# Optimization experiments

Hardware: AMD Instinct MI355X
Metric: run time of the kernel (lower is better)

Reference implementation:

```python
import jax, jax.numpy as jnp
import numpy as np

EMB = 512       # emb_dim
H = 8           # n_heads
HD = EMB // H   # head_dim = 64
FREQ = 64       # freq_features
PERIOD = 0.1
N = 2048


def setup_inputs() -> dict:
    key = jax.random.key(0)
    ks = jax.random.split(key, 6)
    x = jax.random.normal(ks[0], (1, N, EMB), dtype=jnp.float32)
    v = jax.random.normal(ks[1], (1, N, 3), dtype=jnp.float32)
    vec_map = v / jnp.linalg.norm(v, axis=-1, keepdims=True)  # unit direction vectors
    s_in = 1.0 / np.sqrt(EMB)
    W_qkv = jax.random.normal(ks[2], (EMB, 3 * EMB), dtype=jnp.float32) * s_in
    b_qkv = jnp.zeros((3 * EMB,), dtype=jnp.float32)
    W_bias = jax.random.normal(ks[3], (FREQ, H), dtype=jnp.float32) * (1.0 / np.sqrt(FREQ))
    b_bias = jnp.zeros((H,), dtype=jnp.float32)
    W_out = jax.random.normal(ks[4], (EMB, EMB), dtype=jnp.float32) * s_in
    b_out = jnp.zeros((EMB,), dtype=jnp.float32)
    return {"x": x, "vec_map": vec_map, "W_qkv": W_qkv, "b_qkv": b_qkv,
            "W_bias": W_bias, "b_bias": b_bias, "W_out": W_out, "b_out": b_out}


def reference(x, vec_map, W_qkv, b_qkv, W_bias, b_bias, W_out, b_out):
    batch_dim = x.shape[:-2]
    n = x.shape[-2]
    # QKV projection -> (*, N, H, 3, HD)
    qkv = (x @ W_qkv + b_qkv).reshape(*batch_dim, n, H, 3, HD)
    q, k, v = (qkv[..., 0, :], qkv[..., 1, :], qkv[..., 2, :])
    # attention scores (*, Q, K, H), softmax over the K axis (axis=-2)
    attn = jnp.einsum('...qht,...kht->...qkh', q, k) / np.sqrt(HD)
    attn = jax.nn.softmax(attn, axis=-2)
    # relative bias from pairwise angles between direction vectors
    dot = jnp.einsum('...nc,...mc->...nm', vec_map, vec_map)
    angle = jnp.arccos(jnp.clip(dot, 0.0, 1.0)) / 0.001
    freqs = jnp.linspace(0.0, 1.0, FREQ // 2, dtype=jnp.float32) / PERIOD
    phase = freqs * angle[..., None]                      # (*, N, N, FREQ/2)
    pos = jnp.concatenate((jnp.sin(phase), jnp.cos(phase)), axis=-1)  # (*, N, N, FREQ)
    bias = pos @ W_bias + b_bias                          # (*, N, N, H)
    attn = attn + bias
    # weighted sum of values -> (*, N, EMB)
    y = jnp.einsum('...qkh,...kht->...qht', attn, v).reshape(*batch_dim, n, EMB)
    return y @ W_out + b_out
```

## Files before the change

kernel.cpp:

```cpp
#include <hip/hip_runtime.h>
#include <hip/hip_bf16.h>
#include <math.h>

#define NT 2048
#define EMBD 512
#define NH 8
#define QKV_LD 1536
#define KSPLIT 8

typedef unsigned short u16;
typedef __attribute__((ext_vector_type(8))) short short8;
typedef __attribute__((ext_vector_type(4))) float v4f;

static __device__ __forceinline__ float bf2f(unsigned int u) {
    union { unsigned int i; float f; } c; c.i = u << 16; return c.f;
}
static __device__ __forceinline__ unsigned int f2bf(float x) {
    union { float f; unsigned int u; } c; c.f = x;
    return (c.u + 0x7fffu + ((c.u >> 16) & 1u)) >> 16;
}
static __device__ __forceinline__ unsigned int cvtpk(float lo, float hi) {
    unsigned int r;
    asm("v_cvt_pk_bf16_f32 %0, %1, %2" : "=v"(r) : "v"(lo), "v"(hi));
    return r;
}

__global__ __launch_bounds__(256) void prep(const float* __restrict__ x,
    u16* __restrict__ xh, u16* __restrict__ xl,
    const float* __restrict__ Wqkv, u16* __restrict__ wth, u16* __restrict__ wtl,
    const float* __restrict__ Wout, u16* __restrict__ woth, u16* __restrict__ wotl)
{
    __shared__ float tile[64][65];
    int b = blockIdx.x;
    const int t = threadIdx.x;
    if (b < 1024) {
        int i = (b * 256 + t) << 2;
        float4 v = *(const float4*)(x + i);
        float f[4] = {v.x, v.y, v.z, v.w};
        unsigned int hi[4], lo[4];
#pragma unroll
        for (int j = 0; j < 4; ++j) {
            hi[j] = f2bf(f[j]);
            lo[j] = f2bf(f[j] - bf2f(hi[j]));
        }
        uint2 wh; wh.x = hi[0] | (hi[1] << 16); wh.y = hi[2] | (hi[3] << 16);
        uint2 wl; wl.x = lo[0] | (lo[1] << 16); wl.y = lo[2] | (lo[3] << 16);
        *(uint2*)(xh + i) = wh;
        *(uint2*)(xl + i) = wl;
        return;
    }
    b -= 1024;
    const float* W; u16* th; u16* tl; int ld, bx, by;
    if (b < 192) { W = Wqkv; th = wth;  tl = wtl;  ld = QKV_LD; bx = b % 24; by = b / 24; }
    else { b -= 192; W = Wout; th = woth; tl = wotl; ld = EMBD; bx = b & 7; by = b >> 3; }
    const int n0 = bx << 6, k0 = by << 6;
    const int r = t >> 2, c4 = (t & 3) << 4;
#pragma unroll
    for (int j = 0; j < 4; ++j)
        *(float4*)&tile[r][c4 + (j << 2)] =
            *(const float4*)(W + (size_t)(k0 + r) * ld + n0 + c4 + (j << 2));
    __syncthreads();
    const int n_l = t >> 2;
    u16 vh[16], vl[16];
#pragma unroll
    for (int j = 0; j < 16; ++j) {
        float f = tile[c4 + j][n_l];
        unsigned int h = f2bf(f);
        vh[j] = (u16)h;
        vl[j] = (u16)f2bf(f - bf2f(h));
    }
    u16* dh = th + (size_t)(n0 + n_l) * EMBD + k0 + c4;
    u16* dl = tl + (size_t)(n0 + n_l) * EMBD + k0 + c4;
    *(uint4*)dh       = *(uint4*)&vh[0];
    *(uint4*)(dh + 8) = *(uint4*)&vh[8];
    *(uint4*)dl       = *(uint4*)&vl[0];
    *(uint4*)(dl + 8) = *(uint4*)&vl[8];
}

__global__ __launch_bounds__(256) void gemm_qkv_mfma(const u16* __restrict__ xh,
    const u16* __restrict__ xl, const u16* __restrict__ wth,
    const u16* __restrict__ wtl, const float* __restrict__ bias,
    u16* __restrict__ qkvb)
{
    const int n0 = blockIdx.x << 6, m0 = blockIdx.y << 6;
    const int w = threadIdx.x >> 6, lane = threadIdx.x & 63;
    const int wm = w >> 1, wn = w & 1;
    const int fr = lane & 15, kd = (lane >> 4) << 3;

    const u16* ah0 = xh + (size_t)(m0 + wm * 32 + fr) * EMBD + kd;
    const u16* al0 = xl + (size_t)(m0 + wm * 32 + fr) * EMBD + kd;
    const u16* bh0 = wth + (size_t)(n0 + wn * 32 + fr) * EMBD + kd;
    const u16* bl0 = wtl + (size_t)(n0 + wn * 32 + fr) * EMBD + kd;

    v4f acc[2][2] = {};
    for (int kc = 0; kc < EMBD; kc += 32) {
        short8 a_h[2], a_l[2], b_h[2], b_l[2];
#pragma unroll
        for (int im = 0; im < 2; ++im) {
            a_h[im] = *(const short8*)(ah0 + (size_t)im * 16 * EMBD + kc);
            a_l[im] = *(const short8*)(al0 + (size_t)im * 16 * EMBD + kc);
        }
#pragma unroll
        for (int in = 0; in < 2; ++in) {
            b_h[in] = *(const short8*)(bh0 + (size_t)in * 16 * EMBD + kc);
            b_l[in] = *(const short8*)(bl0 + (size_t)in * 16 * EMBD + kc);
        }
#pragma unroll
        for (int im = 0; im < 2; ++im)
#pragma unroll
            for (int in = 0; in < 2; ++in) {
                acc[im][in] = __builtin_amdgcn_mfma_f32_16x16x32_bf16(a_h[im], b_h[in], acc[im][in], 0, 0, 0);
                acc[im][in] = __builtin_amdgcn_mfma_f32_16x16x32_bf16(a_h[im], b_l[in], acc[im][in], 0, 0, 0);
                acc[im][in] = __builtin_amdgcn_mfma_f32_16x16x32_bf16(a_l[im], b_h[in], acc[im][in], 0, 0, 0);
            }
    }
    const int qr = (lane >> 4) << 2;
#pragma unroll
    for (int im = 0; im < 2; ++im)
#pragma unroll
        for (int in = 0; in < 2; ++in) {
            int n = n0 + wn * 32 + in * 16 + fr;
            float bv = bias[n];
#pragma unroll
            for (int r = 0; r < 4; ++r) {
                int m = m0 + wm * 32 + im * 16 + qr + r;
                qkvb[(size_t)m * QKV_LD + n] = (u16)f2bf(acc[im][in][r] + bv);
            }
        }
}

__global__ __launch_bounds__(256) void transpose_v(const u16* __restrict__ qkvb,
                                                   u16* __restrict__ Vt)
{
    __shared__ u16 tile[64][72];
    const int h = blockIdx.y, k0 = blockIdx.x << 6;
    const int t = threadIdx.x;
    {
        int r = t >> 2, cg = (t & 3) << 4;
        const u16* src = qkvb + (size_t)(k0 + r) * QKV_LD + h * 192 + 128 + cg;
        *(uint4*)&tile[r][cg]     = *(const uint4*)src;
        *(uint4*)&tile[r][cg + 8] = *(const uint4*)(src + 8);
    }
    __syncthreads();
    {
        int c = t >> 2, kg = (t & 3) << 4;
        u16 tmp[16];
#pragma unroll
        for (int j = 0; j < 16; ++j) tmp[j] = tile[kg + j][c];
        u16* dst = Vt + ((size_t)h * 64 + c) * NT + k0 + kg;
        *(uint4*)dst       = *(uint4*)&tmp[0];
        *(uint4*)(dst + 8) = *(uint4*)&tmp[8];
    }
}

__global__ __launch_bounds__(512, 2) void attn_pv(
    const u16* __restrict__ qkvb, const u16* __restrict__ Vt,
    float* __restrict__ zpart, float* __restrict__ partsP)
{
    __shared__ u16 tile[8 * 2056];

    const int bid = blockIdx.x;
    const int zsp = bid & 7;
    const int qt  = bid >> 3;
    const int q0 = qt << 5;
    const int kbase = zsp << 8;

    const int t = threadIdx.x;
    const int w = t >> 6;
    const int lane = t & 63;
    const int fr = lane & 15;
    const int hi4 = lane >> 4;
    const int kd = hi4 << 3;
    const int qr = hi4 << 2;

    short8 aq[2][2];
#pragma unroll
    for (int mb = 0; mb < 2; ++mb)
#pragma unroll
        for (int kk = 0; kk < 2; ++kk)
            aq[mb][kk] = *(const short8*)(qkvb +
                (size_t)(q0 + mb * 16 + fr) * QKV_LD + w * 192 + kk * 32 + kd);

    v4f accP[2][4] = {};
    float zacc[2][4] = {};

    const u16* vsrc = Vt + (size_t)(w * 64 + fr) * NT + kd;
    const u16* ksrc = qkvb + (size_t)fr * QKV_LD + w * 192 + 64 + kd;

#define LOADCH(VB, BK, KC)                                                     \
    _Pragma("unroll")                                                          \
    for (int nt = 0; nt < 4; ++nt)                                             \
        _Pragma("unroll")                                                      \
        for (int kk = 0; kk < 2; ++kk) {                                       \
            VB[nt][kk] = *(const short8*)(vsrc + (size_t)nt * 16 * NT +        \
                                          (KC) + kk * 32);                     \
            BK[nt][kk] = *(const short8*)(ksrc + (size_t)((KC) + nt * 16) *    \
                                          QKV_LD + kk * 32);                   \
        }

#define COMPUTECH(VB, BK)                                                      \
    {                                                                          \
        v4f sacc[2][4] = {};                                                   \
        _Pragma("unroll")                                                      \
        for (int mb = 0; mb < 2; ++mb)                                         \
            _Pragma("unroll")                                                  \
            for (int nt = 0; nt < 4; ++nt) {                                   \
                sacc[mb][nt] = __builtin_amdgcn_mfma_f32_16x16x32_bf16(        \
                    aq[mb][0], BK[nt][0], sacc[mb][nt], 0, 0, 0);              \
                sacc[mb][nt] = __builtin_amdgcn_mfma_f32_16x16x32_bf16(        \
                    aq[mb][1], BK[nt][1], sacc[mb][nt], 0, 0, 0);              \
            }                                                                  \
        unsigned int pk[2][4][2];                                              \
        _Pragma("unroll")                                                      \
        for (int mb = 0; mb < 2; ++mb)                                         \
            _Pragma("unroll")                                                  \
            for (int nt = 0; nt < 4; ++nt)                                     \
                _Pragma("unroll")                                              \
                for (int r2 = 0; r2 < 2; ++r2) {                               \
                    float e0 = __expf(sacc[mb][nt][2 * r2] * 0.125f);          \
                    float e1 = __expf(sacc[mb][nt][2 * r2 + 1] * 0.125f);      \
                    zacc[mb][2 * r2] += e0;                                    \
                    zacc[mb][2 * r2 + 1] += e1;                                \
                    pk[mb][nt][r2] = cvtpk(e0, e1);                            \
                }                                                              \
        _Pragma("unroll")                                                      \
        for (int mb = 0; mb < 2; ++mb)                                         \
            _Pragma("unroll")                                                  \
            for (int nt = 0; nt < 4; ++nt) {                                   \
                const int kg = (nt << 1) + (fr >> 3);                          \
                _Pragma("unroll")                                              \
                for (int r = 0; r < 4; ++r) {                                  \
                    const int q = mb * 16 + qr + r;                            \
                    tile[w * 2056 + q * 64 + ((kg ^ (q & 7)) << 3) +           \
                         (fr & 7)] =                                           \
                        (u16)(pk[mb][nt][r >> 1] >> ((r & 1) << 4));           \
                }                                                              \
            }                                                                  \
        _Pragma("unroll")                                                      \
        for (int mb = 0; mb < 2; ++mb) {                                       \
            const int q = mb * 16 + fr;                                        \
            _Pragma("unroll")                                                  \
            for (int kk = 0; kk < 2; ++kk) {                                   \
                short8 ap = *(const short8*)&tile[w * 2056 + q * 64 +          \
                    (((kk * 4 + hi4) ^ (q & 7)) << 3)];                        \
                _Pragma("unroll")                                              \
                for (int nt = 0; nt < 4; ++nt)                                 \
                    accP[mb][nt] = __builtin_amdgcn_mfma_f32_16x16x32_bf16(    \
                        ap, VB[nt][kk], accP[mb][nt], 0, 0, 0);                \
            }                                                                  \
        }                                                                      \
    }

    short8 v0[4][2], b0[4][2], v1[4][2], b1[4][2];
    LOADCH(v0, b0, kbase)
#pragma unroll
    for (int cc = 0; cc < 2; ++cc) {
        LOADCH(v1, b1, kbase + ((2 * cc + 1) << 6))
        COMPUTECH(v0, b0)
        if (cc < 1) { LOADCH(v0, b0, kbase + ((2 * cc + 2) << 6)) }
        COMPUTECH(v1, b1)
    }
#undef LOADCH
#undef COMPUTECH

#pragma unroll
    for (int off = 1; off < 16; off <<= 1)
#pragma unroll
        for (int mb = 0; mb < 2; ++mb)
#pragma unroll
            for (int r = 0; r < 4; ++r)
                zacc[mb][r] += __shfl_xor(zacc[mb][r], off);
    if (fr == 0) {
#pragma unroll
        for (int mb = 0; mb < 2; ++mb)
#pragma unroll
            for (int r = 0; r < 4; ++r)
                zpart[((size_t)zsp * 8 + w) * NT + q0 + mb * 16 + qr + r] = zacc[mb][r];
    }
    float* pP = partsP + (size_t)zsp * NT * EMBD;
#pragma unroll
    for (int mb = 0; mb < 2; ++mb)
#pragma unroll
        for (int nt = 0; nt < 4; ++nt)
#pragma unroll
            for (int r = 0; r < 4; ++r)
                pP[(size_t)(q0 + mb * 16 + qr + r) * EMBD +
                   (w << 6) + (nt << 4) + fr] = accP[mb][nt][r];
}

__global__ __launch_bounds__(512, 4) void bias_v(
    const u16* __restrict__ Vt, const float* __restrict__ vec,
    const float* __restrict__ Wb, const float* __restrict__ bb,
    float* __restrict__ partsB)
{
    __shared__ float flds[32];
    __shared__ float vql[96];
    __shared__ float ang[32 * 65];
    __shared__ u16 tile[8 * 2056];

    const int bid = blockIdx.x;
    const int zsp = bid & 7;
    const int qt  = bid >> 3;
    const int q0 = qt << 5;
    const int kbase = zsp << 8;

    const int t = threadIdx.x;
    const int w = t >> 6;
    const int lane = t & 63;
    const int fr = lane & 15;
    const int hi4 = lane >> 4;
    const int kd = hi4 << 3;
    const int qr = hi4 << 2;

    if (t < 32) flds[t] = __fdiv_rn(__fdiv_rn((float)t, 31.0f), 0.1f);
    else if (t < 128) vql[t - 32] = vec[q0 * 3 + (t - 32)];

    short8 BS, BC;
#pragma unroll
    for (int j = 0; j < 8; ++j) {
        float ws = (fr < 8) ? Wb[(kd + j) * 8 + fr] : 0.0f;
        float wc = (fr < 8) ? Wb[(32 + kd + j) * 8 + fr] : 0.0f;
        BS[j] = (short)f2bf(ws);
        BC[j] = (short)f2bf(wc);
    }
    const float bbv = (fr < 8) ? bb[fr] : 0.0f;

    v4f accB[2][4] = {};

    __syncthreads();

    for (int c = 0; c < 4; ++c) {
        const int kc = kbase + (c << 6);
        {
            const int p0 = t << 2;
            const int q = p0 >> 6;
            const int kl = p0 & 63;
            const float a0 = vql[q * 3], a1 = vql[q * 3 + 1], a2 = vql[q * 3 + 2];
            const float* vk = vec + (size_t)(kc + kl) * 3;
#pragma unroll
            for (int j = 0; j < 4; ++j) {
                float c0 = vk[j * 3], c1 = vk[j * 3 + 1], c2 = vk[j * 3 + 2];
                float dot = __fadd_rn(__fadd_rn(__fmul_rn(a0, c0), __fmul_rn(a1, c1)),
                                      __fmul_rn(a2, c2));
                float dotc = fminf(fmaxf(dot, 0.0f), 1.0f);
                ang[q * 65 + kl + j] = __fdiv_rn(acosf(dotc), 0.001f);
            }
        }
        __syncthreads();
#pragma unroll
        for (int gi = 0; gi < 16; ++gi) {
            const int g = w + (gi << 3);
            const int q = g >> 2;
            const int ksub = (g & 3) << 4;
            const float av = ang[q * 65 + ksub + fr];
            float sv[8], cv[8];
#pragma unroll
            for (int j = 0; j < 8; ++j) {
                float ph = __fmul_rn(flds[kd + j], av);
                float rv = ph * 0.15915494309189535f;
                float rf = rv - floorf(rv);
                sv[j] = __builtin_amdgcn_sinf(rf);
                cv[j] = __builtin_amdgcn_cosf(rf);
            }
            union { uint4 u; short8 v; } As, Ac;
            As.u.x = cvtpk(sv[0], sv[1]); As.u.y = cvtpk(sv[2], sv[3]);
            As.u.z = cvtpk(sv[4], sv[5]); As.u.w = cvtpk(sv[6], sv[7]);
            Ac.u.x = cvtpk(cv[0], cv[1]); Ac.u.y = cvtpk(cv[2], cv[3]);
            Ac.u.z = cvtpk(cv[4], cv[5]); Ac.u.w = cvtpk(cv[6], cv[7]);
            v4f cb = {};
            cb = __builtin_amdgcn_mfma_f32_16x16x32_bf16(As.v, BS, cb, 0, 0, 0);
            cb = __builtin_amdgcn_mfma_f32_16x16x32_bf16(Ac.v, BC, cb, 0, 0, 0);
            if (fr < 8) {
                const int kg = (ksub + qr) >> 3;
                uint2 wv;
                wv.x = cvtpk(cb[0] + bbv, cb[1] + bbv);
                wv.y = cvtpk(cb[2] + bbv, cb[3] + bbv);
                *(uint2*)&tile[fr * 2056 + q * 64 + ((kg ^ (q & 7)) << 3) + (qr & 7)] = wv;
            }
        }
        __syncthreads();
#pragma unroll
        for (int kk = 0; kk < 2; ++kk) {
            const int q0l = 0 * 16 + fr, q1l = 1 * 16 + fr;
            short8 ab0 = *(const short8*)&tile[w * 2056 + q0l * 64 +
                (((kk * 4 + hi4) ^ (q0l & 7)) << 3)];
            short8 ab1 = *(const short8*)&tile[w * 2056 + q1l * 64 +
                (((kk * 4 + hi4) ^ (q1l & 7)) << 3)];
#pragma unroll
            for (int nt = 0; nt < 4; ++nt) {
                short8 vbx = *(const short8*)(Vt +
                    (size_t)(w * 64 + nt * 16 + fr) * NT + kc + kk * 32 + kd);
                accB[0][nt] = __builtin_amdgcn_mfma_f32_16x16x32_bf16(ab0, vbx, accB[0][nt], 0, 0, 0);
                accB[1][nt] = __builtin_amdgcn_mfma_f32_16x16x32_bf16(ab1, vbx, accB[1][nt], 0, 0, 0);
            }
        }
    }
    float* pB = partsB + (size_t)zsp * NT * EMBD;
#pragma unroll
    for (int mb = 0; mb < 2; ++mb)
#pragma unroll
        for (int nt = 0; nt < 4; ++nt)
#pragma unroll
            for (int r = 0; r < 4; ++r)
                pB[(size_t)(q0 + mb * 16 + qr + r) * EMBD +
                   (w << 6) + (nt << 4) + fr] = accB[mb][nt][r];
}

__global__ __launch_bounds__(256) void reduce_y2(const float* __restrict__ partsP,
    const float* __restrict__ partsB, const float* __restrict__ zpart,
    u16* __restrict__ yh, u16* __restrict__ yl)
{
    const int MN = NT * EMBD;
    int i = (blockIdx.x * 256 + threadIdx.x) << 2;
    const int q = i >> 9;
    const int h = (i & 511) >> 6;
    float zs = 0.0f;
#pragma unroll
    for (int z = 0; z < KSPLIT; ++z) zs += zpart[((size_t)z * 8 + h) * NT + q];
    float4 aP = *(const float4*)(partsP + i);
    float4 aB = *(const float4*)(partsB + i);
#pragma unroll
    for (int z = 1; z < KSPLIT; ++z) {
        float4 p = *(const float4*)(partsP + (size_t)z * MN + i);
        float4 b = *(const float4*)(partsB + (size_t)z * MN + i);
        aP.x += p.x; aP.y += p.y; aP.z += p.z; aP.w += p.w;
        aB.x += b.x; aB.y += b.y; aB.z += b.z; aB.w += b.w;
    }
    const float iz = 1.0f / zs;
    float f[4] = {aP.x * iz + aB.x, aP.y * iz + aB.y,
                  aP.z * iz + aB.z, aP.w * iz + aB.w};
    unsigned int hi[4], lo[4];
#pragma unroll
    for (int j = 0; j < 4; ++j) {
        hi[j] = f2bf(f[j]);
        lo[j] = f2bf(f[j] - bf2f(hi[j]));
    }
    uint2 wh; wh.x = hi[0] | (hi[1] << 16); wh.y = hi[2] | (hi[3] << 16);
    uint2 wl; wl.x = lo[0] | (lo[1] << 16); wl.y = lo[2] | (lo[3] << 16);
    *(uint2*)(yh + i) = wh;
    *(uint2*)(yl + i) = wl;
}

__global__ __launch_bounds__(256) void gemm_out_mfma(const u16* __restrict__ yh,
    const u16* __restrict__ yl, const u16* __restrict__ wh,
    const u16* __restrict__ wl, const float* __restrict__ bias,
    float* __restrict__ out)
{
    const int n0 = blockIdx.x << 6, m0 = blockIdx.y << 6;
    const int w = threadIdx.x >> 6, lane = threadIdx.x & 63;
    const int wm = w >> 1, wn = w & 1;
    const int fr = lane & 15, kd = (lane >> 4) << 3;

    const u16* ah0 = yh + (size_t)(m0 + wm * 32 + fr) * EMBD + kd;
    const u16* al0 = yl + (size_t)(m0 + wm * 32 + fr) * EMBD + kd;
    const u16* bh0 = wh + (size_t)(n0 + wn * 32 + fr) * EMBD + kd;
    const u16* bl0 = wl + (size_t)(n0 + wn * 32 + fr) * EMBD + kd;

    v4f acc[2][2] = {};
    for (int kc = 0; kc < EMBD; kc += 32) {
        short8 a_h[2], a_l[2], b_h[2], b_l[2];
#pragma unroll
        for (int im = 0; im < 2; ++im) {
            a_h[im] = *(const short8*)(ah0 + (size_t)im * 16 * EMBD + kc);
            a_l[im] = *(const short8*)(al0 + (size_t)im * 16 * EMBD + kc);
        }
#pragma unroll
        for (int in = 0; in < 2; ++in) {
            b_h[in] = *(const short8*)(bh0 + (size_t)in * 16 * EMBD + kc);
            b_l[in] = *(const short8*)(bl0 + (size_t)in * 16 * EMBD + kc);
        }
#pragma unroll
        for (int im = 0; im < 2; ++im)
#pragma unroll
            for (int in = 0; in < 2; ++in) {
                acc[im][in] = __builtin_amdgcn_mfma_f32_16x16x32_bf16(a_h[im], b_h[in], acc[im][in], 0, 0, 0);
                acc[im][in] = __builtin_amdgcn_mfma_f32_16x16x32_bf16(a_h[im], b_l[in], acc[im][in], 0, 0, 0);
                acc[im][in] = __builtin_amdgcn_mfma_f32_16x16x32_bf16(a_l[im], b_h[in], acc[im][in], 0, 0, 0);
            }
    }
    const int qr = (lane >> 4) << 2;
#pragma unroll
    for (int im = 0; im < 2; ++im)
#pragma unroll
        for (int in = 0; in < 2; ++in) {
            int n = n0 + wn * 32 + in * 16 + fr;
            float bv = bias[n];
#pragma unroll
            for (int r = 0; r < 4; ++r) {
                int m = m0 + wm * 32 + im * 16 + qr + r;
                out[(size_t)m * EMBD + n] = acc[im][in][r] + bv;
            }
        }
}

extern "C" void kernel_launch(void* const* d_in, const int* in_sizes, int n_in,
                              void* d_out, int out_size, void* d_ws, size_t ws_size,
                              hipStream_t stream)
{
    const float* x    = (const float*)d_in[0];
    const float* vec  = (const float*)d_in[1];
    const float* Wqkv = (const float*)d_in[2];
    const float* bqkv = (const float*)d_in[3];
    const float* Wb   = (const float*)d_in[4];
    const float* bb   = (const float*)d_in[5];
    const float* Wout = (const float*)d_in[6];
    const float* bout = (const float*)d_in[7];
    float* out = (float*)d_out;

    char* ws = (char*)d_ws;
    u16*   qkvb   = (u16*)(ws);
    u16*   Vt     = (u16*)(ws + 6291456);
    float* zpart  = (float*)(ws + 8388608);
    float* partsP = (float*)(ws + 8912896);
    float* partsB = (float*)(ws + 42467328);
    u16*   yh     = (u16*)(ws + 76021760);
    u16*   yl     = (u16*)(ws + 78118912);
    u16*   xh     = (u16*)(ws + 80216064);
    u16*   xl     = (u16*)(ws + 82313216);
    u16*   wth    = (u16*)(ws + 84410368);
    u16*   wtl    = (u16*)(ws + 85983232);
    u16*   woth   = (u16*)(ws + 87556096);
    u16*   wotl   = (u16*)(ws + 88080384);

    prep<<<1280, 256, 0, stream>>>(x, xh, xl, Wqkv, wth, wtl, Wout, woth, wotl);
    gemm_qkv_mfma<<<dim3(24, 32), 256, 0, stream>>>(xh, xl, wth, wtl, bqkv, qkvb);
    transpose_v<<<dim3(32, 8), 256, 0, stream>>>(qkvb, Vt);
    bias_v<<<64 * KSPLIT, 512, 0, stream>>>(Vt, vec, Wb, bb, partsB);
    attn_pv<<<64 * KSPLIT, 512, 0, stream>>>(qkvb, Vt, zpart, partsP);
    reduce_y2<<<1024, 256, 0, stream>>>(partsP, partsB, zpart, yh, yl);
    gemm_out_mfma<<<dim3(8, 32), 256, 0, stream>>>(yh, yl, woth, wotl, bout, out);
}
```

Baseline: 243.6 us.

## Fuse V transpose into QKV GEMM epilogue and double-buffer bias_v tiles

The QKV GEMM epilogue now also writes the V columns transposed into Vt, which removes the separate transpose_v kernel launch and its reread of qkvb. In bias_v, each warp computes only the angles it will consume itself into a per-warp LDS slice, and the bias tile is double-buffered. Together these drop two of the three block barriers per chunk. Frequency constants are computed in registers instead of shared memory. The cost is uncoalesced strided 2-byte stores to Vt in the GEMM epilogue, redundant per-lane loads of the query vector, and twice the bias-tile LDS, which may lower occupancy.

After: 248.1 us. About the same (+1.8%).

```diff
diff --git a/kernel.cpp b/kernel.cpp
--- a/kernel.cpp
+++ b/kernel.cpp
@@ -80,9 +80,10 @@
 __global__ __launch_bounds__(256) void gemm_qkv_mfma(const u16* __restrict__ xh,
     const u16* __restrict__ xl, const u16* __restrict__ wth,
     const u16* __restrict__ wtl, const float* __restrict__ bias,
-    u16* __restrict__ qkvb)
-{
-    const int n0 = blockIdx.x << 6, m0 = blockIdx.y << 6;
+    u16* __restrict__ qkvb, u16* __restrict__ Vt)
+{
+    const int bx = blockIdx.x;
+    const int n0 = bx << 6, m0 = blockIdx.y << 6;
     const int w = threadIdx.x >> 6, lane = threadIdx.x & 63;
     const int wm = w >> 1, wn = w & 1;
     const int fr = lane & 15, kd = (lane >> 4) << 3;
@@ -115,42 +116,24 @@
             }
     }
     const int qr = (lane >> 4) << 2;
+    const int isv = ((bx % 3) == 2);
+    const int h = bx / 3;
 #pragma unroll
     for (int im = 0; im < 2; ++im)
 #pragma unroll
         for (int in = 0; in < 2; ++in) {
-            int n = n0 + wn * 32 + in * 16 + fr;
+            int nl = wn * 32 + in * 16 + fr;
+            int n = n0 + nl;
             float bv = bias[n];
 #pragma unroll
             for (int r = 0; r < 4; ++r) {
                 int m = m0 + wm * 32 + im * 16 + qr + r;
-                qkvb[(size_t)m * QKV_LD + n] = (u16)f2bf(acc[im][in][r] + bv);
-            }
-        }
-}
-
-__global__ __launch_bounds__(256) void transpose_v(const u16* __restrict__ qkvb,
-                                                   u16* __restrict__ Vt)
-{
-    __shared__ u16 tile[64][72];
-    const int h = blockIdx.y, k0 = blockIdx.x << 6;
-    const int t = threadIdx.x;
-    {
-        int r = t >> 2, cg = (t & 3) << 4;
-        const u16* src = qkvb + (size_t)(k0 + r) * QKV_LD + h * 192 + 128 + cg;
-        *(uint4*)&tile[r][cg]     = *(const uint4*)src;
-        *(uint4*)&tile[r][cg + 8] = *(const uint4*)(src + 8);
-    }
-    __syncthreads();
-    {
-        int c = t >> 2, kg = (t & 3) << 4;
-        u16 tmp[16];
-#pragma unroll
-        for (int j = 0; j < 16; ++j) tmp[j] = tile[kg + j][c];
-        u16* dst = Vt + ((size_t)h * 64 + c) * NT + k0 + kg;
-        *(uint4*)dst       = *(uint4*)&tmp[0];
-        *(uint4*)(dst + 8) = *(uint4*)&tmp[8];
-    }
+                u16 val = (u16)f2bf(acc[im][in][r] + bv);
+                qkvb[(size_t)m * QKV_LD + n] = val;
+                if (isv)
+                    Vt[((size_t)h * 64 + nl) * NT + m] = val;
+            }
+        }
 }
 
 __global__ __launch_bounds__(512, 2) void attn_pv(
@@ -293,10 +276,8 @@
     const float* __restrict__ Wb, const float* __restrict__ bb,
     float* __restrict__ partsB)
 {
-    __shared__ float flds[32];
-    __shared__ float vql[96];
-    __shared__ float ang[32 * 65];
-    __shared__ u16 tile[8 * 2056];
+    __shared__ float angw[8 * 260];
+    __shared__ u16 tile[2][8 * 2056];
 
     const int bid = blockIdx.x;
     const int zsp = bid & 7;
@@ -312,8 +293,10 @@
     const int kd = hi4 << 3;
     const int qr = hi4 << 2;
 
-    if (t < 32) flds[t] = __fdiv_rn(__fdiv_rn((float)t, 31.0f), 0.1f);
-    else if (t < 128) vql[t - 32] = vec[q0 * 3 + (t - 32)];
+    float fl[8];
+#pragma unroll
+    for (int j = 0; j < 8; ++j)
+        fl[j] = __fdiv_rn(__fdiv_rn((float)(kd + j), 31.0f), 0.1f);
 
     short8 BS, BC;
 #pragma unroll
@@ -327,36 +310,38 @@
 
     v4f accB[2][4] = {};
 
-    __syncthreads();
-
+#pragma unroll
     for (int c = 0; c < 4; ++c) {
         const int kc = kbase + (c << 6);
+        u16* tp = tile[c & 1];
         {
-            const int p0 = t << 2;
-            const int q = p0 >> 6;
-            const int kl = p0 & 63;
-            const float a0 = vql[q * 3], a1 = vql[q * 3 + 1], a2 = vql[q * 3 + 2];
-            const float* vk = vec + (size_t)(kc + kl) * 3;
-#pragma unroll
-            for (int j = 0; j < 4; ++j) {
-                float c0 = vk[j * 3], c1 = vk[j * 3 + 1], c2 = vk[j * 3 + 2];
+#pragma unroll
+            for (int jj = 0; jj < 4; ++jj) {
+                const int idx = (lane << 2) + jj;
+                const int gi = idx >> 4;
+                const int g = w + (gi << 3);
+                const int q = g >> 2;
+                const int kl = ((g & 3) << 4) + (idx & 15);
+                const float* vq = vec + (size_t)(q0 + q) * 3;
+                const float* vk = vec + (size_t)(kc + kl) * 3;
+                float a0 = vq[0], a1 = vq[1], a2 = vq[2];
+                float c0 = vk[0], c1 = vk[1], c2 = vk[2];
                 float dot = __fadd_rn(__fadd_rn(__fmul_rn(a0, c0), __fmul_rn(a1, c1)),
                                       __fmul_rn(a2, c2));
                 float dotc = fminf(fmaxf(dot, 0.0f), 1.0f);
-                ang[q * 65 + kl + j] = __fdiv_rn(acosf(dotc), 0.001f);
-            }
-        }
-        __syncthreads();
+                angw[w * 260 + idx] = __fdiv_rn(acosf(dotc), 0.001f);
+            }
+        }
 #pragma unroll
         for (int gi = 0; gi < 16; ++gi) {
             const int g = w + (gi << 3);
             const int q = g >> 2;
             const int ksub = (g & 3) << 4;
-            const float av = ang[q * 65 + ksub + fr];
+            const float av = angw[w * 260 + (gi << 4) + fr];
             float sv[8], cv[8];
 #pragma unroll
             for (int j = 0; j < 8; ++j) {
-                float ph = __fmul_rn(flds[kd + j], av);
+                float ph = __fmul_rn(fl[j], av);
                 float rv = ph * 0.15915494309189535f;
                 float rf = rv - floorf(rv);
                 sv[j] = __builtin_amdgcn_sinf(rf);
@@ -375,16 +360,16 @@
                 uint2 wv;
                 wv.x = cvtpk(cb[0] + bbv, cb[1] + bbv);
                 wv.y = cvtpk(cb[2] + bbv, cb[3] + bbv);
-                *(uint2*)&tile[fr * 2056 + q * 64 + ((kg ^ (q & 7)) << 3) + (qr & 7)] = wv;
+                *(uint2*)&tp[fr * 2056 + q * 64 + ((kg ^ (q & 7)) << 3) + (qr & 7)] = wv;
             }
         }
         __syncthreads();
 #pragma unroll
         for (int kk = 0; kk < 2; ++kk) {
             const int q0l = 0 * 16 + fr, q1l = 1 * 16 + fr;
-            short8 ab0 = *(const short8*)&tile[w * 2056 + q0l * 64 +
+            short8 ab0 = *(const short8*)&tp[w * 2056 + q0l * 64 +
                 (((kk * 4 + hi4) ^ (q0l & 7)) << 3)];
-            short8 ab1 = *(const short8*)&tile[w * 2056 + q1l * 64 +
+            short8 ab1 = *(const short8*)&tp[w * 2056 + q1l * 64 +
                 (((kk * 4 + hi4) ^ (q1l & 7)) << 3)];
 #pragma unroll
             for (int nt = 0; nt < 4; ++nt) {
@@ -523,8 +508,7 @@
     u16*   wotl   = (u16*)(ws + 88080384);
 
     prep<<<1280, 256, 0, stream>>>(x, xh, xl, Wqkv, wth, wtl, Wout, woth, wotl);
-    gemm_qkv_mfma<<<dim3(24, 32), 256, 0, stream>>>(xh, xl, wth, wtl, bqkv, qkvb);
-    transpose_v<<<dim3(32, 8), 256, 0, stream>>>(qkvb, Vt);
+    gemm_qkv_mfma<<<dim3(24, 32), 256, 0, stream>>>(xh, xl, wth, wtl, bqkv, qkvb, Vt);
     bias_v<<<64 * KSPLIT, 512, 0, stream>>>(Vt, vec, Wb, bb, partsB);
     attn_pv<<<64 * KSPLIT, 512, 0, stream>>>(qkvb, Vt, zpart, partsP);
     reduce_y2<<<1024, 256, 0, stream>>>(partsP, partsB, zpart, yh, yl);
```

## Make angle buffer per-wave and double-buffer bias tile to drop barriers

Applied to the files above, without the earlier changes.

Each wave now computes the angles it will itself consume into a private per-wave LDS slice, so the block-wide barrier between angle computation and sin/cos+MFMA bias generation is removed. The bias tile is double-buffered by chunk parity, which removes the trailing barrier that protected the tile from being overwritten before the next chunk. This cuts two of three barriers per chunk but doubles tile LDS (about 33KB extra), which may reduce occupancy under the 512x4 launch bound.

After: 242.9 us. About the same (-0.3%).

```diff
diff --git a/kernel.cpp b/kernel.cpp
--- a/kernel.cpp
+++ b/kernel.cpp
@@ -295,8 +295,8 @@
 {
     __shared__ float flds[32];
     __shared__ float vql[96];
-    __shared__ float ang[32 * 65];
-    __shared__ u16 tile[8 * 2056];
+    __shared__ float angw[8 * 260];
+    __shared__ u16 tile[2][8 * 2056];
 
     const int bid = blockIdx.x;
     const int zsp = bid & 7;
@@ -331,28 +331,28 @@
 
     for (int c = 0; c < 4; ++c) {
         const int kc = kbase + (c << 6);
-        {
-            const int p0 = t << 2;
-            const int q = p0 >> 6;
-            const int kl = p0 & 63;
+        u16* tp = tile[c & 1];
+#pragma unroll
+        for (int jj = 0; jj < 4; ++jj) {
+            const int idx = lane + (jj << 6);
+            const int gi = idx >> 4;
+            const int g = w + (gi << 3);
+            const int q = g >> 2;
+            const int kl = ((g & 3) << 4) + (idx & 15);
             const float a0 = vql[q * 3], a1 = vql[q * 3 + 1], a2 = vql[q * 3 + 2];
             const float* vk = vec + (size_t)(kc + kl) * 3;
-#pragma unroll
-            for (int j = 0; j < 4; ++j) {
-                float c0 = vk[j * 3], c1 = vk[j * 3 + 1], c2 = vk[j * 3 + 2];
-                float dot = __fadd_rn(__fadd_rn(__fmul_rn(a0, c0), __fmul_rn(a1, c1)),
-                                      __fmul_rn(a2, c2));
-                float dotc = fminf(fmaxf(dot, 0.0f), 1.0f);
-                ang[q * 65 + kl + j] = __fdiv_rn(acosf(dotc), 0.001f);
-            }
-        }
-        __syncthreads();
+            float c0 = vk[0], c1 = vk[1], c2 = vk[2];
+            float dot = __fadd_rn(__fadd_rn(__fmul_rn(a0, c0), __fmul_rn(a1, c1)),
+                                  __fmul_rn(a2, c2));
+            float dotc = fminf(fmaxf(dot, 0.0f), 1.0f);
+            angw[w * 260 + idx] = __fdiv_rn(acosf(dotc), 0.001f);
+        }
 #pragma unroll
         for (int gi = 0; gi < 16; ++gi) {
             const int g = w + (gi << 3);
             const int q = g >> 2;
             const int ksub = (g & 3) << 4;
-            const float av = ang[q * 65 + ksub + fr];
+            const float av = angw[w * 260 + (gi << 4) + fr];
             float sv[8], cv[8];
 #pragma unroll
             for (int j = 0; j < 8; ++j) {
@@ -375,16 +375,16 @@
                 uint2 wv;
                 wv.x = cvtpk(cb[0] + bbv, cb[1] + bbv);
                 wv.y = cvtpk(cb[2] + bbv, cb[3] + bbv);
-                *(uint2*)&tile[fr * 2056 + q * 64 + ((kg ^ (q & 7)) << 3) + (qr & 7)] = wv;
+                *(uint2*)&tp[fr * 2056 + q * 64 + ((kg ^ (q & 7)) << 3) + (qr & 7)] = wv;
             }
         }
         __syncthreads();
 #pragma unroll
         for (int kk = 0; kk < 2; ++kk) {
             const int q0l = 0 * 16 + fr, q1l = 1 * 16 + fr;
-            short8 ab0 = *(const short8*)&tile[w * 2056 + q0l * 64 +
+            short8 ab0 = *(const short8*)&tp[w * 2056 + q0l * 64 +
                 (((kk * 4 + hi4) ^ (q0l & 7)) << 3)];
-            short8 ab1 = *(const short8*)&tile[w * 2056 + q1l * 64 +
+            short8 ab1 = *(const short8*)&tp[w * 2056 + q1l * 64 +
                 (((kk * 4 + hi4) ^ (q1l & 7)) << 3)];
 #pragma unroll
             for (int nt = 0; nt < 4; ++nt) {
```
